# Performance work log

Hardware: AMD Instinct MI355X
Metric: run time of the kernel (lower is better)

Reference implementation:

```python
import jax, jax.numpy as jnp
import numpy as np

# NTU RGB+D 25-joint skeleton edges (1-based)
NTU_EDGES = [(1,2),(2,21),(3,21),(4,3),(5,21),(6,5),(7,6),(8,7),(9,21),(10,9),
             (11,10),(12,11),(13,1),(14,13),(15,14),(16,15),(17,1),(18,17),
             (19,18),(20,19),(22,23),(23,8),(24,25),(25,12)]
NUM_SCALES = 13
NUM_POINT = 25


def build_A_powers(num_scales=NUM_SCALES, v=NUM_POINT):
    # MS-G3D disentangled multi-scale aggregation: exact-k-hop adjacencies, each
    # with self loops, symmetrically normalized, stacked along dim 0 -> (K*V, V).
    A = np.zeros((v, v))
    for i, j in NTU_EDGES:
        A[i - 1, j - 1] = 1.0
        A[j - 1, i - 1] = 1.0
    I = np.eye(v)
    mats = []
    for k in range(num_scales):
        if k == 0:
            Ak = I.copy()
        else:
            Ak = np.minimum(np.linalg.matrix_power(A + I, k), 1) \
               - np.minimum(np.linalg.matrix_power(A + I, k - 1), 1)
            Ak = Ak + I  # with_self=True
        d = Ak.sum(-1)
        dinv = np.where(d > 0, d ** -0.5, 0.0)
        mats.append((dinv[:, None] * Ak) * dinv[None, :])
    return np.concatenate(mats, 0).astype(np.float32)


def batchnorm(x, g, b, axes, ch_axis, eps=1e-5):
    # torch BatchNorm in training mode: biased batch stats + affine
    mean = jnp.mean(x, axes, keepdims=True)
    var = jnp.mean((x - mean) ** 2, axes, keepdims=True)
    shape = [1] * x.ndim
    shape[ch_axis] = -1
    return (x - mean) * jax.lax.rsqrt(var + eps) * g.reshape(shape) + b.reshape(shape)


def ms_gcn(x, A_powers, A_res, W, b, g, beta, num_scales):
    # x: (N, C, T, V); A: (K*V, V)
    A = A_powers + A_res
    support = jnp.einsum('vu,nctu->nctv', A, x)            # (N, C, T, K*V)
    N, C, T, KV = support.shape
    V = KV // num_scales
    support = support.reshape(N, C, T, num_scales, V).transpose(0, 3, 1, 2, 4)
    support = support.reshape(N, num_scales * C, T, V)     # (N, K*C, T, V)
    out = jnp.einsum('oc,nctv->notv', W, support) + b[None, :, None, None]  # 1x1 conv
    out = batchnorm(out, g, beta, (0, 2, 3), 1)
    return jax.nn.relu(out)


def lstm(x, Wih, Whh, bih, bhh):
    # single-layer batch_first LSTM, zero initial state; torch gate order i,f,g,o
    B = x.shape[0]
    H = Whh.shape[1]
    xp = jnp.einsum('bsd,hd->bsh', x, Wih) + bih + bhh     # precompute input proj

    def step(carry, xt):
        h, c = carry
        gates = xt + h @ Whh.T
        i, f, g, o = jnp.split(gates, 4, axis=-1)
        c = jax.nn.sigmoid(f) * c + jax.nn.sigmoid(i) * jnp.tanh(g)
        h = jax.nn.sigmoid(o) * jnp.tanh(c)
        return (h, c), h

    init = (jnp.zeros((B, H), x.dtype), jnp.zeros((B, H), x.dtype))
    _, ys = jax.lax.scan(step, init, jnp.swapaxes(xp, 0, 1))
    return jnp.swapaxes(ys, 0, 1)                          # (B, S, H)


def logsig_rnn(x, n_segments, Wih, Whh, bih, bhh):
    # x: (B, T, d). Depth-2 log-signature per time segment + segment start point,
    # concatenated and fed to an LSTM (Logsig-RNN layer).
    B, T, d = x.shape
    t_vec = np.array([int(round(float(v))) for v in np.linspace(1, T, n_segments + 1)])
    starts = t_vec[:-1] - 1
    ends = t_vec[1:] - 1
    L = int((ends - starts).max()) + 1
    # pad segments to fixed length by repeating the last point (zero increments)
    idx = np.minimum(starts[:, None] + np.arange(L)[None, :], ends[:, None])  # (S, L)
    pts = x[:, idx, :]                                     # (B, S, L, d)
    rel = pts - pts[:, :, :1, :]
    inc = rel[:, :, -1, :]                                 # level-1: total increment
    dx = pts[:, :, 1:, :] - pts[:, :, :-1, :]
    Mm = jnp.einsum('bsli,bslj->bsij', rel[:, :, :-1, :], dx)
    iu, ju = np.triu_indices(d, k=1)
    levy = 0.5 * (Mm[:, :, iu, ju] - Mm[:, :, ju, iu])     # level-2 (Lyndon basis)
    feats = jnp.concatenate([x[:, starts, :], inc, levy], axis=-1)
    return lstm(feats, Wih, Whh, bih, bhh)


def setup_inputs() -> dict:
    key = jax.random.key(0)
    ks = iter(jax.random.split(key, 16))
    N, C, T, V, M = 2, 3, 100, 25, 2
    c1, c2, num_class, K = 96, 192, 60, NUM_SCALES

    def randn(shape, scale):
        return jax.random.normal(next(ks), shape, jnp.float32) * scale

    ls1 = c1 + c1 * (c1 - 1) // 2     # 4656
    ls2 = c2 + c2 * (c2 - 1) // 2     # 18528
    in1 = c1 + ls1                    # 4752
    in2 = c2 + ls2                    # 18720
    Ap = jnp.asarray(build_A_powers())
    return {
        'x': jax.random.normal(next(ks), (N, C, T, V, M), jnp.float32),
        'length': jax.random.randint(next(ks), (N,), 0, T),
        'data_bn_g': jnp.ones((M * V * C,)), 'data_bn_b': jnp.zeros((M * V * C,)),
        'A_powers1': Ap,
        'A_res1': jax.random.uniform(next(ks), Ap.shape, jnp.float32, -1e-6, 1e-6),
        'W1': randn((c1, K * C), (K * C) ** -0.5), 'b1': jnp.zeros((c1,)),
        'bn1_g': jnp.ones((c1,)), 'bn1_b': jnp.zeros((c1,)),
        'Wih1': randn((4 * c1, in1), in1 ** -0.5), 'Whh1': randn((4 * c1, c1), c1 ** -0.5),
        'bih1': jnp.zeros((4 * c1,)), 'bhh1': jnp.zeros((4 * c1,)),
        'bnseg1_g': jnp.ones((50,)), 'bnseg1_b': jnp.zeros((50,)),
        'A_powers2': Ap,
        'A_res2': jax.random.uniform(next(ks), Ap.shape, jnp.float32, -1e-6, 1e-6),
        'W2': randn((c2, K * c1), (K * c1) ** -0.5), 'b2': jnp.zeros((c2,)),
        'bn2_g': jnp.ones((c2,)), 'bn2_b': jnp.zeros((c2,)),
        'Wih2': randn((4 * c2, in2), in2 ** -0.5), 'Whh2': randn((4 * c2, c2), c2 ** -0.5),
        'bih2': jnp.zeros((4 * c2,)), 'bhh2': jnp.zeros((4 * c2,)),
        'bnseg2_g': jnp.ones((30,)), 'bnseg2_b': jnp.zeros((30,)),
        'fcW': randn((num_class, c2), c2 ** -0.5), 'fcb': jnp.zeros((num_class,)),
    }


def reference(x, length, data_bn_g, data_bn_b, A_powers1, A_res1, W1, b1, bn1_g, bn1_b,
              Wih1, Whh1, bih1, bhh1, bnseg1_g, bnseg1_b, A_powers2, A_res2, W2, b2,
              bn2_g, bn2_b, Wih2, Whh2, bih2, bhh2, bnseg2_g, bnseg2_b, fcW, fcb):
    # `length` is accepted but unused, as in the original forward.
    N, C, T, V, M = x.shape
    K = A_powers1.shape[0] // V
    c1, c2 = W1.shape[0], W2.shape[0]
    S1, S2 = 50, 30

    h = x.transpose(0, 4, 3, 1, 2).reshape(N, M * V * C, T)
    h = batchnorm(h, data_bn_g, data_bn_b, (0, 2), 1)
    h = h.reshape(N * M, V, C, T).transpose(0, 2, 3, 1)            # (NM, C, T, V)

    h = jax.nn.relu(ms_gcn(h, A_powers1, A_res1, W1, b1, bn1_g, bn1_b, K))
    h = h.transpose(0, 3, 2, 1).reshape(N * M * V, T, c1)
    h = logsig_rnn(h, S1, Wih1, Whh1, bih1, bhh1)                  # (NMV, S1, c1)
    h = batchnorm(h, bnseg1_g, bnseg1_b, (0, 2), 1)
    h = h.reshape(N * M, V, S1, c1).transpose(0, 3, 2, 1)          # (NM, c1, S1, V)

    h = jax.nn.relu(ms_gcn(h, A_powers2, A_res2, W2, b2, bn2_g, bn2_b, K))
    h = h.transpose(0, 3, 2, 1).reshape(N * M * V, S1, c2)
    h = logsig_rnn(h, S2, Wih2, Whh2, bih2, bhh2)                  # (NMV, S2, c2)
    h = batchnorm(h, bnseg2_g, bnseg2_b, (0, 2), 1)
    h = h.reshape(N * M, V, S2, c2).transpose(0, 3, 2, 1)          # (NM, c2, S2, V)

    pooled = h.reshape(N, M, c2, -1).mean(axis=3).mean(axis=1)     # (N, c2)
    return pooled @ fcW.T + fcb
```

## Files before the change

### kernel.cpp

```cpp
#include <hip/hip_runtime.h>
#include <cmath>
#include <cstdint>
#include <cstddef>

typedef unsigned short bf16_t;
typedef __attribute__((ext_vector_type(8))) short short8;
typedef __attribute__((ext_vector_type(4))) float floatx4;
typedef __attribute__((ext_vector_type(2))) _Float16 half2_t;

__device__ __forceinline__ float bf2f(bf16_t b){
  unsigned int u = ((unsigned int)b) << 16;
  return __uint_as_float(u);
}
__device__ __forceinline__ bf16_t f2bf(float f){
  unsigned int u = __float_as_uint(f);
  unsigned int r = (u + 0x7fffu + ((u >> 16) & 1u)) >> 16;
  return (bf16_t)r;
}
__device__ __forceinline__ unsigned int f2bf2(float a, float b){
  return (unsigned int)f2bf(a) | ((unsigned int)f2bf(b) << 16);
}
__device__ __forceinline__ float sigf(float x){ return 1.0f / (1.0f + expf(-x)); }

__device__ __forceinline__ float dot2(half2_t a, half2_t b, float c){
#if __has_builtin(__builtin_amdgcn_fdot2)
  return __builtin_amdgcn_fdot2(a, b, c, false);
#else
  return c + (float)a.x * (float)b.x + (float)a.y * (float)b.y;
#endif
}

__device__ __forceinline__ void gload_lds16(const bf16_t* g, bf16_t* lds){
  __builtin_amdgcn_global_load_lds(
      (const __attribute__((address_space(1))) unsigned int*)g,
      (__attribute__((address_space(3))) unsigned int*)lds, 16, 0, 0);
}

__global__ void prep_misc(const float* __restrict__ a1, const float* __restrict__ r1, float* __restrict__ o1,
                          const float* __restrict__ a2, const float* __restrict__ r2, float* __restrict__ o2,
                          const float* __restrict__ bi1, const float* __restrict__ bh1, float* __restrict__ ob1,
                          const float* __restrict__ bi2, const float* __restrict__ bh2, float* __restrict__ ob2,
                          const float* __restrict__ Whh1, half2_t* __restrict__ Wp1,
                          const float* __restrict__ Whh2, half2_t* __restrict__ Wp2,
                          unsigned short* __restrict__ lut1, unsigned short* __restrict__ lut2,
                          float* __restrict__ stats, bf16_t* __restrict__ A2mat){
  int i = blockIdx.x * blockDim.x + threadIdx.x;
  if (i < 8125){ o1[i] = a1[i] + r1[i]; o2[i] = a2[i] + r2[i]; }
  if (i < 384) ob1[i] = bi1[i] + bh1[i];
  if (i < 768) ob2[i] = bi2[i] + bh2[i];
  if (i < 736) stats[i] = 0.f;
  if (i < 18432){
    int t = i % 384, j2 = i / 384;
    half2_t w; w.x = (_Float16)Whh1[(size_t)t * 96 + 2 * j2];
    w.y = (_Float16)Whh1[(size_t)t * 96 + 2 * j2 + 1];
    Wp1[i] = w;
  }
  if (i < 73728){
    int t = i % 768, j2 = i / 768;
    half2_t w; w.x = (_Float16)Whh2[(size_t)t * 192 + 2 * j2];
    w.y = (_Float16)Whh2[(size_t)t * 192 + 2 * j2 + 1];
    Wp2[i] = w;
  }
  if (i < 4560){
    int d = 96, p = i;
    int r = (int)(((2.0 * d - 1.0) - sqrt((2.0 * d - 1.0) * (2.0 * d - 1.0) - 8.0 * (double)p)) * 0.5);
    if (r < 0) r = 0;
    while (r + 1 <= d - 2 && (r + 1) * (d - 1) - ((r + 1) * r) / 2 <= p) ++r;
    while (r > 0 && r * (d - 1) - (r * (r - 1)) / 2 > p) --r;
    int jj = p - (r * (d - 1) - (r * (r - 1)) / 2);
    lut1[p] = (unsigned short)((r << 8) | (r + 1 + jj));
  }
  if (i < 18336){
    int d = 192, p = i;
    int r = (int)(((2.0 * d - 1.0) - sqrt((2.0 * d - 1.0) * (2.0 * d - 1.0) - 8.0 * (double)p)) * 0.5);
    if (r < 0) r = 0;
    while (r + 1 <= d - 2 && (r + 1) * (d - 1) - ((r + 1) * r) / 2 <= p) ++r;
    while (r > 0 && r * (d - 1) - (r * (r - 1)) / 2 > p) --r;
    int jj = p - (r * (d - 1) - (r * (r - 1)) / 2);
    lut2[p] = (unsigned short)((r << 8) | (r + 1 + jj));
  }
  if (i < 160000){
    int row = i >> 5, col = 1248 + (i & 31);
    A2mat[(size_t)row * 1280 + col] = 0;
  }
}

__device__ __forceinline__ void f2bf_seg(const float* in, bf16_t* out, int Kin, int Kout, int li){
  int ko8 = Kout >> 3;
  int r = li / ko8, k8 = (li % ko8) << 3;
  uint4 u;
  if (k8 + 8 <= Kin){
    const float4* p = reinterpret_cast<const float4*>(in + (size_t)r * Kin + k8);
    float4 x0 = p[0], x1 = p[1];
    u.x = f2bf2(x0.x, x0.y); u.y = f2bf2(x0.z, x0.w);
    u.z = f2bf2(x1.x, x1.y); u.w = f2bf2(x1.z, x1.w);
  } else {
    u.x = u.y = u.z = u.w = 0u;
  }
  *reinterpret_cast<uint4*>(out + (size_t)r * Kout + k8) = u;
}

__global__ void f2bf_pad8_3(const float* __restrict__ in1, bf16_t* __restrict__ out1, int Kin1, int Kout1, int c1,
                            const float* __restrict__ in2, bf16_t* __restrict__ out2, int Kin2, int Kout2, int c2,
                            const float* __restrict__ in3, bf16_t* __restrict__ out3, int Kin3, int Kout3, int c3){
  int idx = blockIdx.x * blockDim.x + threadIdx.x;
  if (idx < c1){ f2bf_seg(in1, out1, Kin1, Kout1, idx); return; }
  idx -= c1;
  if (idx < c2){ f2bf_seg(in2, out2, Kin2, Kout2, idx); return; }
  idx -= c2;
  if (idx < c3) f2bf_seg(in3, out3, Kin3, Kout3, idx);
}

__global__ void data_bn_kernel(const float* __restrict__ x, const float* __restrict__ g,
                               const float* __restrict__ bb, float* __restrict__ h1,
                               int N, int C, int T, int V, int M){
  int ch = blockIdx.x;
  int m = ch / (V * C);
  int v = (ch / C) % V;
  int c = ch % C;
  int tid = threadIdx.x;
  int cnt = N * T;
  float s = 0.f, s2 = 0.f;
  for (int i = tid; i < cnt; i += 64){
    int n = i / T, t = i % T;
    float val = x[(((size_t)(n * C + c) * T + t) * V + v) * M + m];
    s += val; s2 += val * val;
  }
  for (int off = 32; off; off >>= 1){ s += __shfl_down(s, off); s2 += __shfl_down(s2, off); }
  s = __shfl(s, 0); s2 = __shfl(s2, 0);
  float mean = s / cnt;
  float rstd = rsqrtf(s2 / cnt - mean * mean + 1e-5f);
  float gg = g[ch], bo = bb[ch];
  for (int i = tid; i < cnt; i += 64){
    int n = i / T, t = i % T;
    float val = x[(((size_t)(n * C + c) * T + t) * V + v) * M + m];
    float y = (val - mean) * rstd * gg + bo;
    h1[((size_t)((n * M + m) * C + c) * T + t) * V + v] = y;
  }
}

__global__ __launch_bounds__(256)
void gcn1_fused(const float* __restrict__ A, const float* __restrict__ h1,
                const float* __restrict__ W1, const float* __restrict__ b1,
                float* __restrict__ y1, float* __restrict__ ssum, float* __restrict__ ssq, int T){
  __shared__ float h[3][25];
  __shared__ float sup[3][325];
  __shared__ float lsum[96], lsq[96];
  int blk = blockIdx.x;
  int nm = blk / T, t = blk % T;
  int tid = threadIdx.x;
  if (tid < 75){
    int c = tid / 25, v = tid % 25;
    h[c][v] = h1[((size_t)(nm * 3 + c) * T + t) * 25 + v];
  }
  if (tid < 96){ lsum[tid] = 0.f; lsq[tid] = 0.f; }
  __syncthreads();
  for (int w = tid; w < 975; w += 256){
    int c = w / 325, ww = w % 325;
    const float* ar = A + ww * 25;
    float acc = 0.f;
    #pragma unroll
    for (int u = 0; u < 25; ++u) acc += ar[u] * h[c][u];
    sup[c][ww] = acc;
  }
  __syncthreads();
  for (int o2 = tid; o2 < 2400; o2 += 256){
    int v = o2 / 96, o = o2 % 96;
    float acc = b1[o];
    #pragma unroll
    for (int k = 0; k < 13; ++k)
      #pragma unroll
      for (int c = 0; c < 3; ++c)
        acc += W1[o * 39 + k * 3 + c] * sup[c][k * 25 + v];
    y1[((size_t)blk * 25 + v) * 96 + o] = acc;
    atomicAdd(&lsum[o], acc);
    atomicAdd(&lsq[o], acc * acc);
  }
  __syncthreads();
  if (tid < 96){ atomicAdd(&ssum[tid], lsum[tid]); atomicAdd(&ssq[tid], lsq[tid]); }
}

struct SegTable { int st[50]; int en[50]; };

__global__ void feats_bn_kernel(const float* __restrict__ ymat, const float* __restrict__ sum,
                                const float* __restrict__ sumsq, const float* __restrict__ g,
                                const float* __restrict__ bb, bf16_t* __restrict__ feats,
                                SegTable segs, const unsigned int* __restrict__ lut32,
                                int T, int d, int S, int L, int pairs, int rowlenP, int R){
  __shared__ float pts[4][192];
  int bs = blockIdx.x;
  int b = bs / S, s = bs % S;
  int nm = b / 25, v = b % 25;
  int st = segs.st[s], en = segs.en[s];
  int nt = blockDim.x, tid = threadIdx.x;
  for (int l = 0; l < L; ++l){
    int t = st + l; if (t > en) t = en;
    const float* yrow = ymat + ((size_t)(nm * T + t) * 25 + v) * d;
    for (int i = tid; i < d; i += nt){
      float mean = sum[i] / R;
      float rstd = rsqrtf(sumsq[i] / R - mean * mean + 1e-5f);
      pts[l][i] = fmaxf((yrow[i] - mean) * rstd * g[i] + bb[i], 0.f);
    }
  }
  __syncthreads();
  unsigned int* frow32 = reinterpret_cast<unsigned int*>(feats + (size_t)bs * rowlenP);
  int d2 = d >> 1;
  for (int i2 = tid; i2 < d2; i2 += nt){
    int i = 2 * i2;
    frow32[i2]      = f2bf2(pts[0][i], pts[0][i + 1]);
    frow32[d2 + i2] = f2bf2(pts[L - 1][i] - pts[0][i], pts[L - 1][i + 1] - pts[0][i + 1]);
  }
  int rowlen2 = (2 * d + pairs) >> 1, rowlenP2 = rowlenP >> 1;
  for (int i = tid + rowlen2; i < rowlenP2; i += nt) frow32[i] = 0;
  int Lm2 = L - 2;
  unsigned int* lrow32 = frow32 + d;
  int pairs2 = pairs >> 1;
  for (int p2 = tid; p2 < pairs2; p2 += nt){
    unsigned int ee = lut32[p2];
    int i0 = (ee >> 8) & 255, j0 = ee & 255;
    int i1 = ee >> 24, j1 = (ee >> 16) & 255;
    float acc0 = 0.f, acc1 = 0.f;
    for (int l = 1; l <= Lm2; ++l){
      float ri = pts[l][i0] - pts[0][i0], rj = pts[l][j0] - pts[0][j0];
      float di = pts[l + 1][i0] - pts[l][i0], dj = pts[l + 1][j0] - pts[l][j0];
      acc0 += ri * dj - rj * di;
      float ri1 = pts[l][i1] - pts[0][i1], rj1 = pts[l][j1] - pts[0][j1];
      float di1 = pts[l + 1][i1] - pts[l][i1], dj1 = pts[l + 1][j1] - pts[l][j1];
      acc1 += ri1 * dj1 - rj1 * di1;
    }
    lrow32[p2] = f2bf2(0.5f * acc0, 0.5f * acc1);
  }
}

__global__ __launch_bounds__(256)
void gemm_mfma_nt_split(const bf16_t* __restrict__ A, const bf16_t* __restrict__ B,
                        float* __restrict__ P, int M, int N, int K){
  __shared__ bf16_t As[128 * 64];
  __shared__ bf16_t Bs[128 * 64];
  const int tid = threadIdx.x;
  const int lane = tid & 63, wv = tid >> 6;
  const int bm = blockIdx.x * 128, bn = blockIdx.y * 128;
  const int wr = (wv >> 1) * 64, wc = (wv & 1) * 64;
  const int m_l = lane & 15, q = lane >> 4;

  const int ksteps = K >> 6;
  const int Z = gridDim.z, z = blockIdx.z;
  const int per = (ksteps + Z - 1) / Z;
  const int ks0 = z * per;
  const int ks1 = (ks0 + per < ksteps) ? ks0 + per : ksteps;

  const int rlane = lane >> 3;
  const int slane = lane & 7;
  const int colc = (slane ^ rlane) * 8;
  const bf16_t* gA[4]; const bf16_t* gB[4];
  bf16_t* lA[4]; bf16_t* lB[4];
  #pragma unroll
  for (int it = 0; it < 4; ++it){
    int c = it * 4 + wv;
    int rowA = bm + c * 8 + rlane; if (rowA > M - 1) rowA = M - 1;
    int rowB = bn + c * 8 + rlane; if (rowB > N - 1) rowB = N - 1;
    gA[it] = A + (size_t)rowA * K + colc;
    gB[it] = B + (size_t)rowB * K + colc;
    lA[it] = &As[c * 512];
    lB[it] = &Bs[c * 512];
  }
  const int sxor = m_l & 7;

  floatx4 acc[4][4] = {};
  for (int ks = ks0; ks < ks1; ++ks){
    int k0 = ks << 6;
    __syncthreads();
    #pragma unroll
    for (int it = 0; it < 4; ++it){
      gload_lds16(gA[it] + k0, lA[it]);
      gload_lds16(gB[it] + k0, lB[it]);
    }
    __syncthreads();
    #pragma unroll
    for (int half = 0; half < 2; ++half){
      const int scol = ((half * 4 + q) ^ sxor) * 8;
      short8 af[4], bfr[4];
      #pragma unroll
      for (int i = 0; i < 4; ++i){
        af[i]  = *reinterpret_cast<const short8*>(&As[(wr + i * 16 + m_l) * 64 + scol]);
        bfr[i] = *reinterpret_cast<const short8*>(&Bs[(wc + i * 16 + m_l) * 64 + scol]);
      }
      #pragma unroll
      for (int mi = 0; mi < 4; ++mi)
        #pragma unroll
        for (int ni = 0; ni < 4; ++ni)
          acc[mi][ni] = __builtin_amdgcn_mfma_f32_16x16x32_bf16(af[mi], bfr[ni], acc[mi][ni], 0, 0, 0);
    }
  }

  float* Pz = P + (size_t)z * M * N;
  #pragma unroll
  for (int mi = 0; mi < 4; ++mi){
    int row0 = bm + wr + mi * 16 + q * 4;
    #pragma unroll
    for (int r = 0; r < 4; ++r){
      int row = row0 + r;
      if (row < M){
        #pragma unroll
        for (int ni = 0; ni < 4; ++ni){
          int col = bn + wc + ni * 16 + m_l;
          if (col < N) Pz[(size_t)row * N + col] = acc[mi][ni][r];
        }
      }
    }
  }
}

__global__ __launch_bounds__(256)
void reduce_split_bias_stats(const float* __restrict__ P, const float* __restrict__ bias,
                             float* __restrict__ out, float* __restrict__ ssum, float* __restrict__ ssq,
                             int MN, int N, int Z){
  __shared__ float lsum[192], lsq[192];
  int tid = threadIdx.x;
  if (tid < 192){ lsum[tid] = 0.f; lsq[tid] = 0.f; }
  __syncthreads();
  int i4 = (blockIdx.x * blockDim.x + tid) * 4;
  if (i4 < MN){
    const float4 bv = *reinterpret_cast<const float4*>(bias + (i4 % N));
    float4 s = bv;
    for (int z = 0; z < Z; ++z){
      const float4 p = *reinterpret_cast<const float4*>(P + (size_t)z * MN + i4);
      s.x += p.x; s.y += p.y; s.z += p.z; s.w += p.w;
    }
    *reinterpret_cast<float4*>(out + i4) = s;
    int c0 = i4 % N;
    atomicAdd(&lsum[c0],     s.x); atomicAdd(&lsq[c0],     s.x * s.x);
    atomicAdd(&lsum[c0 + 1], s.y); atomicAdd(&lsq[c0 + 1], s.y * s.y);
    atomicAdd(&lsum[c0 + 2], s.z); atomicAdd(&lsq[c0 + 2], s.z * s.z);
    atomicAdd(&lsum[c0 + 3], s.w); atomicAdd(&lsq[c0 + 3], s.w * s.w);
  }
  __syncthreads();
  if (tid < 192){ atomicAdd(&ssum[tid], lsum[tid]); atomicAdd(&ssq[tid], lsq[tid]); }
}

template <int H2C, int BLK, int Z>
__global__ __launch_bounds__(BLK)
void lstm_kernel(const float* __restrict__ P, const float* __restrict__ bias,
                 const half2_t* __restrict__ Wp, float* __restrict__ out,
                 float* __restrict__ ssum, float* __restrict__ ssq,
                 int S, int MN){
  constexpr int H = 2 * H2C;
  constexpr int H4 = 4 * H;
  __shared__ _Float16 __attribute__((aligned(16))) hsh[H];
  __shared__ float gv[H4];
  __shared__ float ra[BLK / 64], rb[BLK / 64];
  const int b = blockIdx.x, t = threadIdx.x;
  const int lane = t & 63, wid = t >> 6;
  half2_t w[H2C];
  const half2_t* wp = Wp + t;
  #pragma unroll
  for (int j2 = 0; j2 < H2C; ++j2) w[j2] = wp[(size_t)j2 * H4];
  float cc = 0.f;
  if (t < H) hsh[t] = (_Float16)0.f;
  const float bval = bias[t];
  const size_t base = (size_t)b * S * H4 + t;
  float pv0[Z], pv1[Z];
  #pragma unroll
  for (int z = 0; z < Z; ++z) pv0[z] = P[(size_t)z * MN + base];
  #pragma unroll
  for (int z = 0; z < Z; ++z) pv1[z] = P[(size_t)z * MN + base + H4];
  __syncthreads();
  const half2_t* hp = reinterpret_cast<const half2_t*>(hsh);
  for (int s = 0; s < S; ++s){
    float pvn[Z];
    if (s + 2 < S){
      size_t o2 = base + (size_t)(s + 2) * H4;
      #pragma unroll
      for (int z = 0; z < Z; ++z) pvn[z] = P[(size_t)z * MN + o2];
    }
    float a0 = bval, a1 = 0.f, a2 = 0.f, a3 = 0.f;
    float a4 = 0.f, a5 = 0.f, a6 = 0.f, a7 = 0.f;
    #pragma unroll
    for (int z = 0; z < Z; ++z) a0 += pv0[z];
    #pragma unroll
    for (int j2 = 0; j2 < H2C; j2 += 8){
      a0 = dot2(w[j2],     hp[j2],     a0);
      a1 = dot2(w[j2 + 1], hp[j2 + 1], a1);
      a2 = dot2(w[j2 + 2], hp[j2 + 2], a2);
      a3 = dot2(w[j2 + 3], hp[j2 + 3], a3);
      a4 = dot2(w[j2 + 4], hp[j2 + 4], a4);
      a5 = dot2(w[j2 + 5], hp[j2 + 5], a5);
      a6 = dot2(w[j2 + 6], hp[j2 + 6], a6);
      a7 = dot2(w[j2 + 7], hp[j2 + 7], a7);
    }
    gv[t] = ((a0 + a1) + (a2 + a3)) + ((a4 + a5) + (a6 + a7));
    __syncthreads();
    float gvv = 0.f;
    if (t < H){
      float ig = sigf(gv[t]);
      float fg = sigf(gv[H + t]);
      float gg = tanhf(gv[2 * H + t]);
      float og = sigf(gv[3 * H + t]);
      cc = fg * cc + ig * gg;
      float hh = og * tanhf(cc);
      hsh[t] = (_Float16)hh;
      out[((size_t)b * S + s) * H + t] = hh;
      gvv = hh;
    }
    float q1 = gvv, q2 = gvv * gvv;
    for (int off2 = 32; off2; off2 >>= 1){ q1 += __shfl_down(q1, off2); q2 += __shfl_down(q2, off2); }
    if (lane == 0){ ra[wid] = q1; rb[wid] = q2; }
    __syncthreads();
    if (t == 0){
      float sa = 0.f, sb = 0.f;
      #pragma unroll
      for (int ww = 0; ww < BLK / 64; ++ww){ sa += ra[ww]; sb += rb[ww]; }
      atomicAdd(&ssum[s], sa);
      atomicAdd(&ssq[s], sb);
    }
    #pragma unroll
    for (int z = 0; z < Z; ++z){ pv0[z] = pv1[z]; pv1[z] = pvn[z]; }
  }
}

__global__ void support2_bn(const float* __restrict__ A, const float* __restrict__ lout,
                            const float* __restrict__ ssum, const float* __restrict__ ssq,
                            const float* __restrict__ g, const float* __restrict__ bb,
                            bf16_t* __restrict__ A2mat, int S, int cnt){
  int idx = blockIdx.x * blockDim.x + threadIdx.x;
  int total = 4 * S * 25 * 13 * 96;
  if (idx >= total) return;
  int c = idx % 96;
  int k = (idx / 96) % 13;
  int v = (idx / (96 * 13)) % 25;
  int rs = idx / (96 * 13 * 25);
  int s = rs % S, nm = rs / S;
  float mean = ssum[s] / cnt;
  float rstd = rsqrtf(ssq[s] / cnt - mean * mean + 1e-5f);
  float scale = rstd * g[s];
  float shift = bb[s] - mean * scale;
  const float* ar = A + (k * 25 + v) * 25;
  float acc = 0.f;
  #pragma unroll
  for (int u = 0; u < 25; ++u){
    float raw = lout[((size_t)(nm * 25 + u) * S + s) * 96 + c];
    acc += ar[u] * (raw * scale + shift);
  }
  A2mat[((size_t)rs * 25 + v) * 1280 + k * 96 + c] = f2bf(acc);
}

__global__ void pool_kernel(const float* __restrict__ lout2, const float* __restrict__ sum,
                            const float* __restrict__ sumsq, const float* __restrict__ g,
                            const float* __restrict__ bb, float* __restrict__ pooled,
                            int S, int H, int scnt){
  int n = blockIdx.x / H;
  int o = blockIdx.x % H;
  float acc = 0.f;
  int cnt = 2 * 25 * S;
  for (int i = threadIdx.x; i < cnt; i += 64){
    int m = i / (25 * S);
    int r = i % (25 * S);
    int v = r / S;
    int s = r % S;
    int b = (n * 2 + m) * 25 + v;
    float val = lout2[((size_t)b * S + s) * H + o];
    float mean = sum[s] / scnt;
    float rstd = rsqrtf(sumsq[s] / scnt - mean * mean + 1e-5f);
    val = (val - mean) * rstd * g[s] + bb[s];
    acc += val;
  }
  for (int off = 32; off; off >>= 1) acc += __shfl_down(acc, off);
  if (threadIdx.x == 0) pooled[n * H + o] = acc / cnt;
}

__global__ void fc_kernel(const float* __restrict__ pooled, const float* __restrict__ fcW,
                          const float* __restrict__ fcb, float* __restrict__ outp){
  int idx = blockIdx.x * blockDim.x + threadIdx.x;
  if (idx >= 120) return;
  int n = idx / 60, cls = idx % 60;
  float acc = fcb[cls];
  for (int o = 0; o < 192; ++o) acc += pooled[n * 192 + o] * fcW[cls * 192 + o];
  outp[idx] = acc;
}

static void make_segs(int T, int S, SegTable& tab, int& L){
  double step = (double)(T - 1) / (double)S;
  long long tv[51];
  for (int i = 0; i <= S; ++i){
    double v = 1.0 + step * (double)i;
    tv[i] = llrint(v);
  }
  L = 0;
  for (int s = 0; s < S; ++s){
    tab.st[s] = (int)tv[s] - 1;
    tab.en[s] = (int)tv[s + 1] - 1;
    int len = tab.en[s] - tab.st[s] + 1;
    if (len > L) L = len;
  }
  for (int s = S; s < 50; ++s){ tab.st[s] = 0; tab.en[s] = 0; }
  if (L > 4) L = 4;
}

extern "C" void kernel_launch(void* const* d_in, const int* in_sizes, int n_in,
                              void* d_out, int out_size, void* d_ws, size_t ws_size,
                              hipStream_t stream){
  const float* x         = (const float*)d_in[0];
  const float* data_bn_g = (const float*)d_in[2];
  const float* data_bn_b = (const float*)d_in[3];
  const float* A_powers1 = (const float*)d_in[4];
  const float* A_res1    = (const float*)d_in[5];
  const float* W1        = (const float*)d_in[6];
  const float* b1        = (const float*)d_in[7];
  const float* bn1_g     = (const float*)d_in[8];
  const float* bn1_b     = (const float*)d_in[9];
  const float* Wih1      = (const float*)d_in[10];
  const float* Whh1      = (const float*)d_in[11];
  const float* bih1      = (const float*)d_in[12];
  const float* bhh1      = (const float*)d_in[13];
  const float* bnseg1_g  = (const float*)d_in[14];
  const float* bnseg1_b  = (const float*)d_in[15];
  const float* A_powers2 = (const float*)d_in[16];
  const float* A_res2    = (const float*)d_in[17];
  const float* W2        = (const float*)d_in[18];
  const float* b2        = (const float*)d_in[19];
  const float* bn2_g     = (const float*)d_in[20];
  const float* bn2_b     = (const float*)d_in[21];
  const float* Wih2      = (const float*)d_in[22];
  const float* Whh2      = (const float*)d_in[23];
  const float* bih2      = (const float*)d_in[24];
  const float* bhh2      = (const float*)d_in[25];
  const float* bnseg2_g  = (const float*)d_in[26];
  const float* bnseg2_b  = (const float*)d_in[27];
  const float* fcW       = (const float*)d_in[28];
  const float* fcb       = (const float*)d_in[29];
  float* out = (float*)d_out;

  const int N = 2, C = 3, T = 100, V = 25, M = 2, NM = 4;
  const int C1 = 96, C2 = 192;
  const int S1 = 50, S2 = 30;
  const int B = 100;
  const int IN1 = 4752, IN2 = 18720;
  const int IN1P = 4800, IN2P = 18752;
  const int P1 = 4560, P2 = 18336;
  const int KG2 = 1248, KG2P = 1280;
  const int Z1 = 5, Z2 = 6, ZG = 4;

  size_t off = 0;
  char* base = (char*)d_ws;
  auto alloc = [&](size_t nbytes) -> void* {
    off = (off + 255) & ~(size_t)255;
    void* p = base + off;
    off += nbytes;
    return p;
  };
  float* A1full = (float*)alloc(325 * 25 * 4);
  float* A2full = (float*)alloc(325 * 25 * 4);
  float* h1     = (float*)alloc((size_t)NM * C * T * V * 4);
  float* y1mat  = (float*)alloc((size_t)NM * T * V * C1 * 4);
  float* stats  = (float*)alloc(736 * 4);
  float* st1a = stats, *st1b = stats + 96;
  float* sg1a = stats + 192, *sg1b = stats + 242;
  float* st2a = stats + 292, *st2b = stats + 484;
  float* sg2a = stats + 676, *sg2b = stats + 706;
  float* l1out  = (float*)alloc((size_t)B * S1 * C1 * 4);
  bf16_t* A2mat = (bf16_t*)alloc((size_t)NM * S1 * V * KG2P * 2);
  float* y2mat  = (float*)alloc((size_t)NM * S1 * V * C2 * 4);
  float* l2out  = (float*)alloc((size_t)B * S2 * C2 * 4);
  float* pooled = (float*)alloc(2 * C2 * 4);
  float* bias1  = (float*)alloc(4 * C1 * 4);
  float* bias2  = (float*)alloc(4 * C2 * 4);
  half2_t* Wp1  = (half2_t*)alloc((size_t)(C1 / 2) * 4 * C1 * 4);
  half2_t* Wp2  = (half2_t*)alloc((size_t)(C2 / 2) * 4 * C2 * 4);
  bf16_t* Wih1b = (bf16_t*)alloc((size_t)4 * C1 * IN1P * 2);
  bf16_t* Wih2b = (bf16_t*)alloc((size_t)4 * C2 * IN2P * 2);
  bf16_t* W2b   = (bf16_t*)alloc((size_t)C2 * KG2P * 2);
  unsigned short* lut1 = (unsigned short*)alloc((size_t)P1 * 2);
  unsigned short* lut2 = (unsigned short*)alloc((size_t)P2 * 2);
  size_t pmax = (size_t)Z2 * 3000 * 768;
  {
    size_t p1s = (size_t)Z1 * 5000 * 384; if (p1s > pmax) pmax = p1s;
    size_t pgs = (size_t)ZG * 5000 * 192; if (pgs > pmax) pmax = pgs;
  }
  float* Pbuf = (float*)alloc(pmax * 4);
  bf16_t* feats = (bf16_t*)alloc((size_t)B * S2 * IN2P * 2);
  (void)ws_size; (void)in_sizes; (void)n_in; (void)out_size;

  prep_misc<<<625, 256, 0, stream>>>(A_powers1, A_res1, A1full, A_powers2, A_res2, A2full,
                                     bih1, bhh1, bias1, bih2, bhh2, bias2,
                                     Whh1, Wp1, Whh2, Wp2, lut1, lut2, stats, A2mat);
  {
    int c1 = 4 * C1 * (IN1P / 8);
    int c2 = 4 * C2 * (IN2P / 8);
    int c3 = C2 * (KG2P / 8);
    int tot = c1 + c2 + c3;
    f2bf_pad8_3<<<(tot + 255) / 256, 256, 0, stream>>>(Wih1, Wih1b, IN1, IN1P, c1,
                                                       Wih2, Wih2b, IN2, IN2P, c2,
                                                       W2, W2b, KG2, KG2P, c3);
  }

  data_bn_kernel<<<M * V * C, 64, 0, stream>>>(x, data_bn_g, data_bn_b, h1, N, C, T, V, M);

  gcn1_fused<<<NM * T, 256, 0, stream>>>(A1full, h1, W1, b1, y1mat, st1a, st1b, T);

  SegTable seg1, seg2; int L1, L2;
  make_segs(T, S1, seg1, L1);
  make_segs(S1, S2, seg2, L2);

  feats_bn_kernel<<<B * S1, 256, 0, stream>>>(y1mat, st1a, st1b, bn1_g, bn1_b, feats, seg1,
                                              (const unsigned int*)lut1, T, C1, S1, L1, P1, IN1P,
                                              NM * T * 25);
  {
    int Mm = B * S1, Nn = 4 * C1;
    dim3 g((Mm + 127) / 128, (Nn + 127) / 128, Z1);
    gemm_mfma_nt_split<<<g, 256, 0, stream>>>(feats, Wih1b, Pbuf, Mm, Nn, IN1P);
    lstm_kernel<48, 384, Z1><<<B, 384, 0, stream>>>(Pbuf, bias1, Wp1, l1out, sg1a, sg1b, S1, Mm * Nn);
  }

  {
    int tot = NM * S1 * 25 * 13 * 96;
    support2_bn<<<(tot + 255) / 256, 256, 0, stream>>>(A2full, l1out, sg1a, sg1b, bnseg1_g,
                                                       bnseg1_b, A2mat, S1, B * C1);
  }
  {
    int Mm = NM * S1 * 25, Nn = C2;
    dim3 g((Mm + 127) / 128, (Nn + 127) / 128, ZG);
    gemm_mfma_nt_split<<<g, 256, 0, stream>>>(A2mat, W2b, Pbuf, Mm, Nn, KG2P);
    int MN = Mm * Nn;
    reduce_split_bias_stats<<<(MN / 4 + 255) / 256, 256, 0, stream>>>(Pbuf, b2, y2mat, st2a, st2b,
                                                                      MN, Nn, ZG);
  }

  feats_bn_kernel<<<B * S2, 256, 0, stream>>>(y2mat, st2a, st2b, bn2_g, bn2_b, feats, seg2,
                                              (const unsigned int*)lut2, S1, C2, S2, L2, P2, IN2P,
                                              NM * S1 * 25);
  {
    int Mm = B * S2, Nn = 4 * C2;
    dim3 g((Mm + 127) / 128, (Nn + 127) / 128, Z2);
    gemm_mfma_nt_split<<<g, 256, 0, stream>>>(feats, Wih2b, Pbuf, Mm, Nn, IN2P);
    lstm_kernel<96, 768, Z2><<<B, 768, 0, stream>>>(Pbuf, bias2, Wp2, l2out, sg2a, sg2b, S2, Mm * Nn);
  }

  pool_kernel<<<2 * C2, 64, 0, stream>>>(l2out, sg2a, sg2b, bnseg2_g, bnseg2_b, pooled, S2, C2, B * C2);
  fc_kernel<<<1, 128, 0, stream>>>(pooled, fcW, fcb, out);
}
```

Before: 679.6 us.

## Add 256x256 eight-phase pipelined MFMA GEMM for second LSTM input projection

Adds a new 512-thread split-K GEMM kernel that uses 256x256 output tiles with double-buffered LDS staged through direct global-to-LDS loads. Each k-step is split into four phases that interleave the next tile's loads with MFMA work, using raw barriers, explicit vmcnt waits and setprio. The second LSTM input projection now runs on this kernel, and split-K rises from 6 to 7 slices. The aim is more reuse per tile and latency hiding for the large K=18752 GEMM. In exchange there are fewer output blocks, heavy LDS and register use per block, and fragile hand-tuned synchronisation.

```diff
diff --git a/kernel.cpp b/kernel.cpp
--- a/kernel.cpp
+++ b/kernel.cpp
@@ -34,6 +34,10 @@
   __builtin_amdgcn_global_load_lds(
       (const __attribute__((address_space(1))) unsigned int*)g,
       (__attribute__((address_space(3))) unsigned int*)lds, 16, 0, 0);
+}
+
+__device__ __forceinline__ void barrier_raw(){
+  asm volatile("s_barrier" ::: "memory");
 }
 
 __global__ void prep_misc(const float* __restrict__ a1, const float* __restrict__ r1, float* __restrict__ o1,
@@ -304,6 +308,111 @@
         #pragma unroll
         for (int ni = 0; ni < 4; ++ni){
           int col = bn + wc + ni * 16 + m_l;
+          if (col < N) Pz[(size_t)row * N + col] = acc[mi][ni][r];
+        }
+      }
+    }
+  }
+}
+
+#define VMC4 asm volatile("s_waitcnt vmcnt(4)" ::: "memory")
+#define VMC0 asm volatile("s_waitcnt vmcnt(0)" ::: "memory")
+#define STG_A8(NB, KH, OFF) { gload_lds16(pA0 + (OFF) + (KH) * 32, dA0 + (NB) * 16384 + (KH) * 8192); \
+                              gload_lds16(pA1 + (OFF) + (KH) * 32, dA1 + (NB) * 16384 + (KH) * 8192); }
+#define STG_B8(NB, KH, OFF) { gload_lds16(pB0 + (OFF) + (KH) * 32, dB0 + (NB) * 16384 + (KH) * 8192); \
+                              gload_lds16(pB1 + (OFF) + (KH) * 32, dB1 + (NB) * 16384 + (KH) * 8192); }
+#define PH8(BUF, KH, MIB, LOADB, STAGE_BLOCK, WAIT_BLOCK) { \
+    const bf16_t* ab_ = As + (BUF) * 16384 + (KH) * 8192 + sA + (MIB) * 512; \
+    _Pragma("unroll") \
+    for (int i_ = 0; i_ < 4; ++i_) af[i_] = *reinterpret_cast<const short8*>(ab_ + i_ * 512); \
+    if (LOADB){ \
+      const bf16_t* bb_ = Bs + (BUF) * 16384 + (KH) * 8192 + sB; \
+      _Pragma("unroll") \
+      for (int i_ = 0; i_ < 4; ++i_) bfr[i_] = *reinterpret_cast<const short8*>(bb_ + i_ * 512); \
+    } \
+    STAGE_BLOCK; \
+    WAIT_BLOCK; \
+    barrier_raw(); \
+    __builtin_amdgcn_s_setprio(1); \
+    _Pragma("unroll") \
+    for (int mi_ = 0; mi_ < 4; ++mi_) \
+      _Pragma("unroll") \
+      for (int ni_ = 0; ni_ < 4; ++ni_) \
+        acc[(MIB) + mi_][ni_] = __builtin_amdgcn_mfma_f32_16x16x32_bf16(af[mi_], bfr[ni_], acc[(MIB) + mi_][ni_], 0, 0, 0); \
+    __builtin_amdgcn_s_setprio(0); \
+    barrier_raw(); \
+  }
+
+__global__ __launch_bounds__(512, 2)
+void gemm_mfma_nt_8ph(const bf16_t* __restrict__ A, const bf16_t* __restrict__ B,
+                      float* __restrict__ P, int M, int N, int K){
+  __shared__ bf16_t As[32768];
+  __shared__ bf16_t Bs[32768];
+  const int tid = threadIdx.x;
+  const int lane = tid & 63, wv = tid >> 6;
+  const int wm = wv >> 2, wn = wv & 3;
+  const int m_l = lane & 15, q = lane >> 4;
+  const int bm = blockIdx.x * 256, bn = blockIdx.y * 256;
+
+  const int ksteps = K >> 6;
+  const int z = blockIdx.z, Z = gridDim.z;
+  const int per = (ksteps + Z - 1) / Z;
+  const int ks0 = z * per;
+  int ks1 = ks0 + per; if (ks1 > ksteps) ks1 = ksteps;
+  if (ks0 >= ks1) return;
+
+  const int rlane = lane >> 2, slane = lane & 3;
+  const int cg = slane ^ (rlane & 3);
+  int rr0 = wv * 16 + rlane, rr1 = (8 + wv) * 16 + rlane;
+  int ra0 = bm + rr0; if (ra0 > M - 1) ra0 = M - 1;
+  int ra1 = bm + rr1; if (ra1 > M - 1) ra1 = M - 1;
+  int rb0 = bn + rr0; if (rb0 > N - 1) rb0 = N - 1;
+  int rb1 = bn + rr1; if (rb1 > N - 1) rb1 = N - 1;
+  const bf16_t* pA0 = A + (size_t)ra0 * K + cg * 8 + ks0 * 64;
+  const bf16_t* pA1 = A + (size_t)ra1 * K + cg * 8 + ks0 * 64;
+  const bf16_t* pB0 = B + (size_t)rb0 * K + cg * 8 + ks0 * 64;
+  const bf16_t* pB1 = B + (size_t)rb1 * K + cg * 8 + ks0 * 64;
+  bf16_t* dA0 = As + wv * 512;
+  bf16_t* dA1 = As + (8 + wv) * 512;
+  bf16_t* dB0 = Bs + wv * 512;
+  bf16_t* dB1 = Bs + (8 + wv) * 512;
+
+  const int sA = (wm * 128 + m_l) * 32 + ((q ^ (m_l & 3)) * 8);
+  const int sB = (wn * 64 + m_l) * 32 + ((q ^ (m_l & 3)) * 8);
+
+  short8 af[4], bfr[4];
+  floatx4 acc[8][4] = {};
+
+  STG_A8(0, 0, 0); STG_B8(0, 0, 0); STG_A8(0, 1, 0); STG_B8(0, 1, 0);
+  VMC4;
+  barrier_raw();
+
+  int buf = 0;
+  for (int t = ks0; t < ks1 - 1; ++t){
+    const int nb = buf ^ 1;
+    PH8(buf, 0, 0, true,  STG_A8(nb, 0, 64), ((void)0));
+    PH8(buf, 0, 4, false, STG_B8(nb, 0, 64), VMC4);
+    PH8(buf, 1, 0, true,  STG_A8(nb, 1, 64), ((void)0));
+    PH8(buf, 1, 4, false, STG_B8(nb, 1, 64), VMC4);
+    pA0 += 64; pA1 += 64; pB0 += 64; pB1 += 64;
+    buf = nb;
+  }
+  PH8(buf, 0, 0, true,  ((void)0), ((void)0));
+  PH8(buf, 0, 4, false, ((void)0), VMC0);
+  PH8(buf, 1, 0, true,  ((void)0), ((void)0));
+  PH8(buf, 1, 4, false, ((void)0), ((void)0));
+
+  float* Pz = P + (size_t)z * M * N;
+  #pragma unroll
+  for (int mi = 0; mi < 8; ++mi){
+    int row0 = bm + wm * 128 + mi * 16 + q * 4;
+    #pragma unroll
+    for (int r = 0; r < 4; ++r){
+      int row = row0 + r;
+      if (row < M){
+        #pragma unroll
+        for (int ni = 0; ni < 4; ++ni){
+          int col = bn + wn * 64 + ni * 16 + m_l;
           if (col < N) Pz[(size_t)row * N + col] = acc[mi][ni][r];
         }
       }
@@ -538,7 +647,7 @@
   const int IN1P = 4800, IN2P = 18752;
   const int P1 = 4560, P2 = 18336;
   const int KG2 = 1248, KG2P = 1280;
-  const int Z1 = 5, Z2 = 6, ZG = 4;
+  const int Z1 = 5, Z2 = 7, ZG = 4;
 
   size_t off = 0;
   char* base = (char*)d_ws;
@@ -630,8 +739,8 @@
                                               NM * S1 * 25);
   {
     int Mm = B * S2, Nn = 4 * C2;
-    dim3 g((Mm + 127) / 128, (Nn + 127) / 128, Z2);
-    gemm_mfma_nt_split<<<g, 256, 0, stream>>>(feats, Wih2b, Pbuf, Mm, Nn, IN2P);
+    dim3 g((Mm + 255) / 256, (Nn + 255) / 256, Z2);
+    gemm_mfma_nt_8ph<<<g, 512, 0, stream>>>(feats, Wih2b, Pbuf, Mm, Nn, IN2P);
     lstm_kernel<96, 768, Z2><<<B, 768, 0, stream>>>(Pbuf, bias2, Wp2, l2out, sg2a, sg2b, S2, Mm * Nn);
   }
 
```

Measured after the change: 676.7 us. No clear change (-0.4%).
